# Optimization experiments

Hardware: AMD Instinct MI355X
Metric: run time of the kernel (lower is better)

The kernel has to match this reference:

```python
import jax, jax.numpy as jnp
import numpy as np

DIM, HEADS, MLP_RATIO = 384, 6, 4.0
HEAD_DIM = DIM // HEADS
HID = int(DIM * MLP_RATIO)
EPS = 1e-5


def _layer_norm(x, g, b):
    m = jnp.mean(x, axis=-1, keepdims=True)
    v = jnp.mean(jnp.square(x - m), axis=-1, keepdims=True)
    return (x - m) * jax.lax.rsqrt(v + EPS) * g + b


def setup_inputs() -> dict:
    key = jax.random.key(0)
    ks = jax.random.split(key, 16)
    B, N, C = 4, 2048, DIM
    s = 0.02
    return {
        "x": jax.random.normal(ks[0], (B, N, C), dtype=jnp.float32),
        "ln1_g": jnp.ones((C,), jnp.float32),
        "ln1_b": jnp.zeros((C,), jnp.float32),
        "qkv_w": jax.random.normal(ks[1], (C, 3 * C), jnp.float32) * s,  # [in, out]
        "qkv_b": jnp.zeros((3 * C,), jnp.float32),
        "proj_w": jax.random.normal(ks[2], (C, C), jnp.float32) * s,
        "proj_b": jnp.zeros((C,), jnp.float32),
        "ln2_g": jnp.ones((C,), jnp.float32),
        "ln2_b": jnp.zeros((C,), jnp.float32),
        "fc1_w": jax.random.normal(ks[3], (C, HID), jnp.float32) * s,
        "fc1_b": jnp.zeros((HID,), jnp.float32),
        "fc2_w": jax.random.normal(ks[4], (HID, C), jnp.float32) * s,
        "fc2_b": jnp.zeros((C,), jnp.float32),
    }


def reference(x, ln1_g, ln1_b, qkv_w, qkv_b, proj_w, proj_b,
              ln2_g, ln2_b, fc1_w, fc1_b, fc2_w, fc2_b):
    B, N, C = x.shape
    scale = HEAD_DIM ** (-0.5)

    # --- attention branch (pre-norm) ---
    h = _layer_norm(x, ln1_g, ln1_b)
    qkv = (h @ qkv_w + qkv_b).reshape(B, N, 3, HEADS, HEAD_DIM)
    qkv = jnp.transpose(qkv, (2, 0, 3, 1, 4))  # [3, B, H, N, D]
    q, k, v = qkv[0], qkv[1], qkv[2]
    attn = jnp.einsum("bhnd,bhmd->bhnm", q, k) * scale
    attn = jax.nn.softmax(attn, axis=-1)
    out = jnp.einsum("bhnm,bhmd->bhnd", attn, v)
    out = jnp.transpose(out, (0, 2, 1, 3)).reshape(B, N, C)
    x = x + (out @ proj_w + proj_b)

    # --- MLP branch (pre-norm) ---
    h = _layer_norm(x, ln2_g, ln2_b)
    h = jax.nn.gelu(h @ fc1_w + fc1_b, approximate=False)
    x = x + (h @ fc2_w + fc2_b)
    return x
```

## Files before the change

kernel.cpp:

```cpp
#include <hip/hip_runtime.h>

typedef unsigned short u16;
typedef unsigned int u32;
typedef __bf16 bf16x8_t __attribute__((ext_vector_type(8)));
typedef float f32x4 __attribute__((ext_vector_type(4)));
typedef float f32x16 __attribute__((ext_vector_type(16)));

__device__ __forceinline__ u16 f2b(float f) {
  union { float f; u32 u; } v; v.f = f;
  u32 r = v.u + 0x7fffu + ((v.u >> 16) & 1u);
  return (u16)(r >> 16);
}

__device__ __forceinline__ u32 pkbf(float a, float b) {
  union { __bf16 h[2]; u32 u; } v;
  v.h[0] = (__bf16)a; v.h[1] = (__bf16)b;
  return v.u;
}

__device__ __forceinline__ f32x4 mfma16(uint4 a, uint4 b, f32x4 c) {
  return __builtin_amdgcn_mfma_f32_16x16x32_bf16(
      __builtin_bit_cast(bf16x8_t, a), __builtin_bit_cast(bf16x8_t, b), c, 0, 0, 0);
}

__device__ __forceinline__ f32x16 mfma32(uint4 a, uint4 b, f32x16 c) {
  return __builtin_amdgcn_mfma_f32_32x32x16_bf16(
      __builtin_bit_cast(bf16x8_t, a), __builtin_bit_cast(bf16x8_t, b), c, 0, 0, 0);
}

__device__ __forceinline__ void plswap(u32& a, u32& b) {
  asm("v_permlane32_swap_b32 %0, %1" : "+v"(a), "+v"(b));
}

__device__ __forceinline__ void load_lds16(const void* g, void* l) {
  __builtin_amdgcn_global_load_lds(
      (const __attribute__((address_space(1))) unsigned int*)g,
      (__attribute__((address_space(3))) unsigned int*)l, 16, 0, 0);
}

__global__ __launch_bounds__(256) void convT4_k(
    const float* __restrict__ w0, u16* __restrict__ t0_,
    const float* __restrict__ w1, u16* __restrict__ t1_,
    const float* __restrict__ w2, u16* __restrict__ t2_,
    const float* __restrict__ w3, u16* __restrict__ t3_) {
  __shared__ u16 L[64][68];
  int tile = blockIdx.x, tid = threadIdx.x;
  const float* w; u16* wt; int K, N, rel;
  if (tile < 108)      { w = w0; wt = t0_; K = 384;  N = 1152; rel = tile; }
  else if (tile < 144) { w = w1; wt = t1_; K = 384;  N = 384;  rel = tile - 108; }
  else if (tile < 288) { w = w2; wt = t2_; K = 384;  N = 1536; rel = tile - 144; }
  else                 { w = w3; wt = t3_; K = 1536; N = 384;  rel = tile - 288; }
  int ntx = N >> 6;
  int tk = (rel / ntx) << 6, tn = (rel - (rel / ntx) * ntx) << 6;

  int r = tid >> 2, c0 = (tid & 3) << 4;
  const float* src = w + (size_t)(tk + r) * N + tn + c0;
#pragma unroll
  for (int j = 0; j < 16; j += 4) {
    float4 a = *(const float4*)(src + j);
    L[r][c0 + j + 0] = f2b(a.x);
    L[r][c0 + j + 1] = f2b(a.y);
    L[r][c0 + j + 2] = f2b(a.z);
    L[r][c0 + j + 3] = f2b(a.w);
  }
  __syncthreads();
  int n = tid >> 2, k0 = (tid & 3) << 4;
  u16 tmp[16];
#pragma unroll
  for (int j = 0; j < 16; j++) tmp[j] = L[k0 + j][n];
  u16* dst = wt + (size_t)(tn + n) * K + tk + k0;
  *(uint4*)dst = *(const uint4*)(tmp);
  *(uint4*)(dst + 8) = *(const uint4*)(tmp + 8);
}

__global__ __launch_bounds__(256) void ln_k(const float* __restrict__ x,
                                            const float* __restrict__ g,
                                            const float* __restrict__ bta,
                                            u16* __restrict__ out) {
  int lane = threadIdx.x & 63, wid = threadIdx.x >> 6;
  int row = blockIdx.x * 4 + wid;
  const float* xr = x + (size_t)row * 384;
  float v[6];
  float s = 0.f;
#pragma unroll
  for (int i = 0; i < 6; i++) { v[i] = xr[i * 64 + lane]; s += v[i]; }
#pragma unroll
  for (int off = 32; off >= 1; off >>= 1) s += __shfl_xor(s, off);
  float mean = s * (1.0f / 384.0f);
  float vs = 0.f;
#pragma unroll
  for (int i = 0; i < 6; i++) { float d = v[i] - mean; vs += d * d; }
#pragma unroll
  for (int off = 32; off >= 1; off >>= 1) vs += __shfl_xor(vs, off);
  float rstd = rsqrtf(vs * (1.0f / 384.0f) + 1e-5f);
  u16* orow = out + (size_t)row * 384;
#pragma unroll
  for (int i = 0; i < 6; i++) {
    int c = i * 64 + lane;
    orow[c] = f2b((v[i] - mean) * rstd * g[c] + bta[c]);
  }
}

template <int EPI, int MR>
__global__ __launch_bounds__(256) void gemm_k(
    const u16* __restrict__ A, const u16* __restrict__ Bt,
    const float* __restrict__ bias, const float* __restrict__ res,
    void* __restrict__ outp, int M, int Nn, int K,
    u16* __restrict__ qp, u16* __restrict__ kp, u16* __restrict__ vtp) {
  constexpr int BMt = MR * 32;
  constexpr int AWV = BMt / 32;
  __shared__ __align__(16) u16 As[2][BMt * 64];
  __shared__ __align__(16) u16 Bs[2][64 * 64];
  int tid = threadIdx.x;
  int lane = tid & 63, wid = tid >> 6;
  int li = lane & 15, lg = lane >> 4;
  int wr = wid >> 1, wc = wid & 1;
  int row0 = blockIdx.y * BMt, col0 = blockIdx.x * 64;

  int lr = lane >> 3;
  int sc8 = ((lane & 7) ^ lr) * 8;

  f32x4 z = {0.f, 0.f, 0.f, 0.f};
  f32x4 acc[MR][2];
#pragma unroll
  for (int m = 0; m < MR; m++)
#pragma unroll
    for (int n = 0; n < 2; n++) acc[m][n] = z;

  auto STAGE = [&](int buf, int k0) {
#pragma unroll
    for (int j = 0; j < AWV; j++) {
      int ia = wid * AWV + j;
      load_lds16(A + (size_t)(row0 + ia * 8 + lr) * K + k0 + sc8,
                 (char*)As[buf] + ia * 1024);
    }
#pragma unroll
    for (int j = 0; j < 2; j++) {
      int ib = wid * 2 + j;
      load_lds16(Bt + (size_t)(col0 + ib * 8 + lr) * K + k0 + sc8,
                 (char*)Bs[buf] + ib * 1024);
    }
  };

  int nsteps = K >> 6;
  STAGE(0, 0);

  int buf = 0;
  for (int t = 0; t < nsteps; t++) {
    if (t + 1 < nsteps) {
      STAGE(buf ^ 1, (t + 1) * 64);
      if constexpr (MR == 4)
        asm volatile("s_waitcnt vmcnt(6)" ::: "memory");
      else
        asm volatile("s_waitcnt vmcnt(4)" ::: "memory");
    } else {
      asm volatile("s_waitcnt vmcnt(0)" ::: "memory");
    }
    __builtin_amdgcn_s_barrier();
    asm volatile("" ::: "memory");
    const char* Asb = (const char*)As[buf];
    const char* Bsb = (const char*)Bs[buf];
#pragma unroll
    for (int kk = 0; kk < 2; kk++) {
      uint4 af[MR], bf[2];
#pragma unroll
      for (int m = 0; m < MR; m++) {
        int r = wr * (MR * 16) + m * 16 + li;
        af[m] = *(const uint4*)(Asb + r * 128 +
                                ((kk * 64 + lg * 16) ^ ((r & 7) << 4)));
      }
#pragma unroll
      for (int n = 0; n < 2; n++) {
        int c = wc * 32 + n * 16 + li;
        bf[n] = *(const uint4*)(Bsb + c * 128 +
                                ((kk * 64 + lg * 16) ^ ((c & 7) << 4)));
      }
#pragma unroll
      for (int m = 0; m < MR; m++)
#pragma unroll
        for (int n = 0; n < 2; n++)
          acc[m][n] = mfma16(af[m], bf[n], acc[m][n]);
    }
    asm volatile("" ::: "memory");
    __builtin_amdgcn_s_barrier();
    buf ^= 1;
  }

#pragma unroll
  for (int m = 0; m < MR; m++) {
#pragma unroll
    for (int n = 0; n < 2; n++) {
#pragma unroll
      for (int j = 0; j < 4; j++) {
        int r = row0 + wr * (MR * 16) + m * 16 + lg * 4 + j;
        int c = col0 + wc * 32 + n * 16 + li;
        float v = acc[m][n][j] + bias[c];
        if (EPI == 0) {
          ((float*)outp)[(size_t)r * Nn + c] = v + res[(size_t)r * Nn + c];
        } else if (EPI == 1) {
          float e = __expf(-1.5957691f * v * (1.f + 0.044715f * v * v));
          ((u16*)outp)[(size_t)r * Nn + c] = f2b(v / (1.f + e));
        } else {
          int t = c / 384;
          int c2 = c - t * 384;
          int hh = c2 >> 6, d = c2 & 63;
          int bb = r >> 11, nn = r & 2047;
          size_t bh = (size_t)bb * 6 + hh;
          int tile = nn >> 5;
          if (t == 2) {
            int kvl = nn & 31;
            int kvHalf = (kvl >> 4) & 1, h2 = (kvl >> 3) & 1, jj = kvl & 7;
            int dTile = d >> 5, l31 = d & 31;
            vtp[(((bh * 64 + tile) * 2 + dTile) * 2 + kvHalf) * 512 +
                (l31 + h2 * 32) * 8 + jj] = f2b(v);
          } else {
            int chunk = d >> 4, h2 = (d >> 3) & 1, e = d & 7;
            int l31 = nn & 31;
            size_t off = ((bh * 64 + tile) * 4 + chunk) * 512 +
                         (l31 + h2 * 32) * 8 + e;
            if (t == 0) qp[off] = f2b(v * 0.125f);
            else        kp[off] = f2b(v);
          }
        }
      }
    }
  }
}

__global__ __launch_bounds__(256, 3) void attn_k(const u16* __restrict__ q,
                                                 const u16* __restrict__ k,
                                                 const u16* __restrict__ vt,
                                                 u16* __restrict__ out) {
  __shared__ __align__(16) float Ol[3][2][16][64];
  __shared__ float Ls[3][64];

  int tid = threadIdx.x;
  int lane = tid & 63, wid = tid >> 6;
  int l31 = lane & 31, hi = lane >> 5;
  int bid = blockIdx.x;
  int nid = (bid & 7) * 192 + (bid >> 3);
  int bh = nid >> 6, qTile = nid & 63;
  int b = bh / 6, hh = bh - b * 6;
  int qb = qTile * 32;

  const u16* qp_ = q + (size_t)(bh * 64 + qTile) * 2048 + lane * 8;
  const u16* kp_ = k + (size_t)(bh * 64 + wid * 16) * 2048 + lane * 8;
  const u16* vp_ = vt + (size_t)(bh * 64 + wid * 16) * 2048 + lane * 8;

  uint4 qf[4], kf[4];
#pragma unroll
  for (int c = 0; c < 4; c++) qf[c] = *(const uint4*)(qp_ + c * 512);
#pragma unroll
  for (int c = 0; c < 4; c++) kf[c] = *(const uint4*)(kp_ + c * 512);
  kp_ += 2048;

  f32x16 o0, o1;
#pragma unroll
  for (int r = 0; r < 16; r++) { o0[r] = 0.f; o1[r] = 0.f; }
  float lsum = 0.f;

#pragma unroll
  for (int t = 0; t < 16; t++) {
    uint4 vf0 = *(const uint4*)(vp_);
    uint4 vf1 = *(const uint4*)(vp_ + 512);
    uint4 vf2 = *(const uint4*)(vp_ + 1024);
    uint4 vf3 = *(const uint4*)(vp_ + 1536);
    uint4 kn[4];
    if (t < 15) {
#pragma unroll
      for (int c = 0; c < 4; c++) kn[c] = *(const uint4*)(kp_ + c * 512);
    }

    f32x16 s;
#pragma unroll
    for (int r = 0; r < 16; r++) s[r] = 0.f;
    s = mfma32(kf[0], qf[0], s);
    s = mfma32(kf[1], qf[1], s);
    s = mfma32(kf[2], qf[2], s);
    s = mfma32(kf[3], qf[3], s);

    float p[16];
#pragma unroll
    for (int r = 0; r < 16; r++) p[r] = __expf(s[r]);

    float a0 = (p[0] + p[1]) + (p[2] + p[3]);
    float a1 = (p[4] + p[5]) + (p[6] + p[7]);
    float a2 = (p[8] + p[9]) + (p[10] + p[11]);
    float a3 = (p[12] + p[13]) + (p[14] + p[15]);
    lsum += (a0 + a1) + (a2 + a3);

    u32 u[8];
#pragma unroll
    for (int i = 0; i < 8; i++) u[i] = pkbf(p[2 * i], p[2 * i + 1]);
    plswap(u[0], u[2]); plswap(u[1], u[3]);
    plswap(u[4], u[6]); plswap(u[5], u[7]);
    uint4 pa0 = {u[0], u[1], u[2], u[3]};
    uint4 pa1 = {u[4], u[5], u[6], u[7]};

    o0 = mfma32(pa0, vf0, o0);
    o0 = mfma32(pa1, vf1, o0);
    o1 = mfma32(pa0, vf2, o1);
    o1 = mfma32(pa1, vf3, o1);

    if (t < 15) {
#pragma unroll
      for (int c = 0; c < 4; c++) kf[c] = kn[c];
    }
    kp_ += 2048;
    vp_ += 2048;
  }

  lsum += __shfl_xor(lsum, 32);

  if (wid) {
#pragma unroll
    for (int r = 0; r < 16; r++) {
      Ol[wid - 1][0][r][lane] = o0[r];
      Ol[wid - 1][1][r][lane] = o1[r];
    }
    Ls[wid - 1][lane] = lsum;
  }
  __syncthreads();
  if (wid == 0) {
#pragma unroll
    for (int w = 0; w < 3; w++) lsum += Ls[w][lane];
#pragma unroll
    for (int r = 0; r < 16; r++)
#pragma unroll
      for (int w = 0; w < 3; w++) {
        o0[r] += Ol[w][0][r][lane];
        o1[r] += Ol[w][1][r][lane];
      }
    float rl = 1.0f / lsum;
#pragma unroll
    for (int r = 0; r < 16; r++) {
      int qo = (r & 3) + 8 * (r >> 2) + hi * 4;
      float rlq = __shfl(rl, qo, 64);
      int row = b * 2048 + qb + qo;
      out[(size_t)row * 384 + hh * 64 + l31] = f2b(o0[r] * rlq);
      out[(size_t)row * 384 + hh * 64 + 32 + l31] = f2b(o1[r] * rlq);
    }
  }
}

extern "C" void kernel_launch(void* const* d_in, const int* in_sizes, int n_in,
                              void* d_out, int out_size, void* d_ws,
                              size_t ws_size, hipStream_t stream) {
  const float* x      = (const float*)d_in[0];
  const float* ln1_g  = (const float*)d_in[1];
  const float* ln1_b  = (const float*)d_in[2];
  const float* qkv_w  = (const float*)d_in[3];
  const float* qkv_b  = (const float*)d_in[4];
  const float* proj_w = (const float*)d_in[5];
  const float* proj_b = (const float*)d_in[6];
  const float* ln2_g  = (const float*)d_in[7];
  const float* ln2_b  = (const float*)d_in[8];
  const float* fc1_w  = (const float*)d_in[9];
  const float* fc1_b  = (const float*)d_in[10];
  const float* fc2_w  = (const float*)d_in[11];
  const float* fc2_b  = (const float*)d_in[12];
  float* out = (float*)d_out;

  char* p = (char*)d_ws;
  u16* qkvwt  = (u16*)p;  p += (size_t)1152 * 384 * 2;
  u16* projwt = (u16*)p;  p += (size_t)384 * 384 * 2;
  u16* fc1wt  = (u16*)p;  p += (size_t)1536 * 384 * 2;
  u16* fc2wt  = (u16*)p;  p += (size_t)384 * 1536 * 2;
  float* x1   = (float*)p; p += (size_t)8192 * 384 * 4;
  u16* reg1   = (u16*)p;  p += (size_t)8192 * 384 * 2;
  u16* reg2   = (u16*)p;  p += (size_t)8192 * 1536 * 2;
  u16* qd  = reg2;
  u16* kd  = reg2 + (size_t)24 * 2048 * 64;
  u16* vtd = kd + (size_t)24 * 2048 * 64;
  u16* h3  = reg2;

  convT4_k<<<432, 256, 0, stream>>>(qkv_w, qkvwt, proj_w, projwt,
                                    fc1_w, fc1wt, fc2_w, fc2wt);

  ln_k<<<2048, 256, 0, stream>>>(x, ln1_g, ln1_b, reg1);
  gemm_k<2, 4><<<dim3(18, 64), 256, 0, stream>>>(
      reg1, qkvwt, qkv_b, nullptr, nullptr, 8192, 1152, 384, qd, kd, vtd);
  attn_k<<<dim3(1536), 256, 0, stream>>>(qd, kd, vtd, reg1);
  gemm_k<0, 2><<<dim3(6, 128), 256, 0, stream>>>(
      reg1, projwt, proj_b, x, x1, 8192, 384, 384, nullptr, nullptr, nullptr);
  ln_k<<<2048, 256, 0, stream>>>(x1, ln2_g, ln2_b, reg1);
  gemm_k<1, 4><<<dim3(24, 64), 256, 0, stream>>>(
      reg1, fc1wt, fc1_b, nullptr, h3, 8192, 1536, 384, nullptr, nullptr, nullptr);
  gemm_k<0, 2><<<dim3(6, 128), 256, 0, stream>>>(
      h3, fc2wt, fc2_b, x1, out, 8192, 384, 1536, nullptr, nullptr, nullptr);
}
```

Before: 140.1 us.

## Widen GEMM N-tiles and process two query tiles per attention block

The GEMM kernel gains an NR template parameter, so the QKV and FC1 GEMMs now use 128x128 tiles instead of 128x64, halving the grid width and the re-reading of A. The attention kernel now handles 64 queries per block (two 32-row tiles) sharing each K/V fragment load, and K and V are prefetched together. It also switches exp to exp2 by folding log2(e) into the Q scale. In exchange the kernels use more registers and drop attention occupancy from 3 to 2 blocks per SM, and the output reduction through shared memory runs twice with extra barriers.

```diff
diff --git a/kernel.cpp b/kernel.cpp
--- a/kernel.cpp
+++ b/kernel.cpp
@@ -36,6 +36,14 @@
   __builtin_amdgcn_global_load_lds(
       (const __attribute__((address_space(1))) unsigned int*)g,
       (__attribute__((address_space(3))) unsigned int*)l, 16, 0, 0);
+}
+
+template <int N>
+__device__ __forceinline__ void waitvm() {
+  if constexpr (N == 0) asm volatile("s_waitcnt vmcnt(0)" ::: "memory");
+  else if constexpr (N == 4) asm volatile("s_waitcnt vmcnt(4)" ::: "memory");
+  else if constexpr (N == 6) asm volatile("s_waitcnt vmcnt(6)" ::: "memory");
+  else asm volatile("s_waitcnt vmcnt(8)" ::: "memory");
 }
 
 __global__ __launch_bounds__(256) void convT4_k(
@@ -101,42 +109,42 @@
   }
 }
 
-template <int EPI, int MR>
+template <int EPI, int MR, int NR>
 __global__ __launch_bounds__(256) void gemm_k(
     const u16* __restrict__ A, const u16* __restrict__ Bt,
     const float* __restrict__ bias, const float* __restrict__ res,
     void* __restrict__ outp, int M, int Nn, int K,
     u16* __restrict__ qp, u16* __restrict__ kp, u16* __restrict__ vtp) {
   constexpr int BMt = MR * 32;
-  constexpr int AWV = BMt / 32;
+  constexpr int BNt = NR * 32;
   __shared__ __align__(16) u16 As[2][BMt * 64];
-  __shared__ __align__(16) u16 Bs[2][64 * 64];
+  __shared__ __align__(16) u16 Bs[2][BNt * 64];
   int tid = threadIdx.x;
   int lane = tid & 63, wid = tid >> 6;
   int li = lane & 15, lg = lane >> 4;
   int wr = wid >> 1, wc = wid & 1;
-  int row0 = blockIdx.y * BMt, col0 = blockIdx.x * 64;
+  int row0 = blockIdx.y * BMt, col0 = blockIdx.x * BNt;
 
   int lr = lane >> 3;
   int sc8 = ((lane & 7) ^ lr) * 8;
 
   f32x4 z = {0.f, 0.f, 0.f, 0.f};
-  f32x4 acc[MR][2];
+  f32x4 acc[MR][NR];
 #pragma unroll
   for (int m = 0; m < MR; m++)
 #pragma unroll
-    for (int n = 0; n < 2; n++) acc[m][n] = z;
+    for (int n = 0; n < NR; n++) acc[m][n] = z;
 
   auto STAGE = [&](int buf, int k0) {
 #pragma unroll
-    for (int j = 0; j < AWV; j++) {
-      int ia = wid * AWV + j;
+    for (int j = 0; j < MR; j++) {
+      int ia = wid * MR + j;
       load_lds16(A + (size_t)(row0 + ia * 8 + lr) * K + k0 + sc8,
                  (char*)As[buf] + ia * 1024);
     }
 #pragma unroll
-    for (int j = 0; j < 2; j++) {
-      int ib = wid * 2 + j;
+    for (int j = 0; j < NR; j++) {
+      int ib = wid * NR + j;
       load_lds16(Bt + (size_t)(col0 + ib * 8 + lr) * K + k0 + sc8,
                  (char*)Bs[buf] + ib * 1024);
     }
@@ -149,12 +157,9 @@
   for (int t = 0; t < nsteps; t++) {
     if (t + 1 < nsteps) {
       STAGE(buf ^ 1, (t + 1) * 64);
-      if constexpr (MR == 4)
-        asm volatile("s_waitcnt vmcnt(6)" ::: "memory");
-      else
-        asm volatile("s_waitcnt vmcnt(4)" ::: "memory");
+      waitvm<MR + NR>();
     } else {
-      asm volatile("s_waitcnt vmcnt(0)" ::: "memory");
+      waitvm<0>();
     }
     __builtin_amdgcn_s_barrier();
     asm volatile("" ::: "memory");
@@ -162,7 +167,7 @@
     const char* Bsb = (const char*)Bs[buf];
 #pragma unroll
     for (int kk = 0; kk < 2; kk++) {
-      uint4 af[MR], bf[2];
+      uint4 af[MR], bf[NR];
 #pragma unroll
       for (int m = 0; m < MR; m++) {
         int r = wr * (MR * 16) + m * 16 + li;
@@ -170,15 +175,15 @@
                                 ((kk * 64 + lg * 16) ^ ((r & 7) << 4)));
       }
 #pragma unroll
-      for (int n = 0; n < 2; n++) {
-        int c = wc * 32 + n * 16 + li;
+      for (int n = 0; n < NR; n++) {
+        int c = wc * (NR * 16) + n * 16 + li;
         bf[n] = *(const uint4*)(Bsb + c * 128 +
                                 ((kk * 64 + lg * 16) ^ ((c & 7) << 4)));
       }
 #pragma unroll
       for (int m = 0; m < MR; m++)
 #pragma unroll
-        for (int n = 0; n < 2; n++)
+        for (int n = 0; n < NR; n++)
           acc[m][n] = mfma16(af[m], bf[n], acc[m][n]);
     }
     asm volatile("" ::: "memory");
@@ -189,11 +194,11 @@
 #pragma unroll
   for (int m = 0; m < MR; m++) {
 #pragma unroll
-    for (int n = 0; n < 2; n++) {
+    for (int n = 0; n < NR; n++) {
 #pragma unroll
       for (int j = 0; j < 4; j++) {
         int r = row0 + wr * (MR * 16) + m * 16 + lg * 4 + j;
-        int c = col0 + wc * 32 + n * 16 + li;
+        int c = col0 + wc * (NR * 16) + n * 16 + li;
         float v = acc[m][n][j] + bias[c];
         if (EPI == 0) {
           ((float*)outp)[(size_t)r * Nn + c] = v + res[(size_t)r * Nn + c];
@@ -218,7 +223,7 @@
             int l31 = nn & 31;
             size_t off = ((bh * 64 + tile) * 4 + chunk) * 512 +
                          (l31 + h2 * 32) * 8 + e;
-            if (t == 0) qp[off] = f2b(v * 0.125f);
+            if (t == 0) qp[off] = f2b(v * 0.18033688f);
             else        kp[off] = f2b(v);
           }
         }
@@ -227,7 +232,7 @@
   }
 }
 
-__global__ __launch_bounds__(256, 3) void attn_k(const u16* __restrict__ q,
+__global__ __launch_bounds__(256, 2) void attn_k(const u16* __restrict__ q,
                                                  const u16* __restrict__ k,
                                                  const u16* __restrict__ vt,
                                                  u16* __restrict__ out) {
@@ -238,107 +243,155 @@
   int lane = tid & 63, wid = tid >> 6;
   int l31 = lane & 31, hi = lane >> 5;
   int bid = blockIdx.x;
-  int nid = (bid & 7) * 192 + (bid >> 3);
-  int bh = nid >> 6, qTile = nid & 63;
+  int nid = (bid & 7) * 96 + (bid >> 3);
+  int bh = nid >> 5, qT = nid & 31;
   int b = bh / 6, hh = bh - b * 6;
-  int qb = qTile * 32;
-
-  const u16* qp_ = q + (size_t)(bh * 64 + qTile) * 2048 + lane * 8;
-  const u16* kp_ = k + (size_t)(bh * 64 + wid * 16) * 2048 + lane * 8;
-  const u16* vp_ = vt + (size_t)(bh * 64 + wid * 16) * 2048 + lane * 8;
-
-  uint4 qf[4], kf[4];
-#pragma unroll
-  for (int c = 0; c < 4; c++) qf[c] = *(const uint4*)(qp_ + c * 512);
+  int qb = qT * 64;
+
+  const u16* qp_ = q + ((size_t)bh * 64 + qT * 2) * 2048 + lane * 8;
+  const u16* kp_ = k + ((size_t)bh * 64 + wid * 16) * 2048 + lane * 8;
+  const u16* vp_ = vt + ((size_t)bh * 64 + wid * 16) * 2048 + lane * 8;
+
+  uint4 qf0[4], qf1[4], kf[4], vf[4];
+#pragma unroll
+  for (int c = 0; c < 4; c++) qf0[c] = *(const uint4*)(qp_ + c * 512);
+#pragma unroll
+  for (int c = 0; c < 4; c++) qf1[c] = *(const uint4*)(qp_ + 2048 + c * 512);
 #pragma unroll
   for (int c = 0; c < 4; c++) kf[c] = *(const uint4*)(kp_ + c * 512);
+#pragma unroll
+  for (int c = 0; c < 4; c++) vf[c] = *(const uint4*)(vp_ + c * 512);
   kp_ += 2048;
-
-  f32x16 o0, o1;
-#pragma unroll
-  for (int r = 0; r < 16; r++) { o0[r] = 0.f; o1[r] = 0.f; }
-  float lsum = 0.f;
+  vp_ += 2048;
+
+  f32x16 o00, o01, o10, o11;
+#pragma unroll
+  for (int r = 0; r < 16; r++) { o00[r] = 0.f; o01[r] = 0.f; o10[r] = 0.f; o11[r] = 0.f; }
+  float ls0 = 0.f, ls1 = 0.f;
 
 #pragma unroll
   for (int t = 0; t < 16; t++) {
-    uint4 vf0 = *(const uint4*)(vp_);
-    uint4 vf1 = *(const uint4*)(vp_ + 512);
-    uint4 vf2 = *(const uint4*)(vp_ + 1024);
-    uint4 vf3 = *(const uint4*)(vp_ + 1536);
-    uint4 kn[4];
+    uint4 kn[4], vn[4];
     if (t < 15) {
 #pragma unroll
       for (int c = 0; c < 4; c++) kn[c] = *(const uint4*)(kp_ + c * 512);
-    }
-
-    f32x16 s;
-#pragma unroll
-    for (int r = 0; r < 16; r++) s[r] = 0.f;
-    s = mfma32(kf[0], qf[0], s);
-    s = mfma32(kf[1], qf[1], s);
-    s = mfma32(kf[2], qf[2], s);
-    s = mfma32(kf[3], qf[3], s);
-
-    float p[16];
-#pragma unroll
-    for (int r = 0; r < 16; r++) p[r] = __expf(s[r]);
-
-    float a0 = (p[0] + p[1]) + (p[2] + p[3]);
-    float a1 = (p[4] + p[5]) + (p[6] + p[7]);
-    float a2 = (p[8] + p[9]) + (p[10] + p[11]);
-    float a3 = (p[12] + p[13]) + (p[14] + p[15]);
-    lsum += (a0 + a1) + (a2 + a3);
-
-    u32 u[8];
-#pragma unroll
-    for (int i = 0; i < 8; i++) u[i] = pkbf(p[2 * i], p[2 * i + 1]);
-    plswap(u[0], u[2]); plswap(u[1], u[3]);
-    plswap(u[4], u[6]); plswap(u[5], u[7]);
-    uint4 pa0 = {u[0], u[1], u[2], u[3]};
-    uint4 pa1 = {u[4], u[5], u[6], u[7]};
-
-    o0 = mfma32(pa0, vf0, o0);
-    o0 = mfma32(pa1, vf1, o0);
-    o1 = mfma32(pa0, vf2, o1);
-    o1 = mfma32(pa1, vf3, o1);
+#pragma unroll
+      for (int c = 0; c < 4; c++) vn[c] = *(const uint4*)(vp_ + c * 512);
+    }
+
+    f32x16 s0, s1;
+#pragma unroll
+    for (int r = 0; r < 16; r++) { s0[r] = 0.f; s1[r] = 0.f; }
+#pragma unroll
+    for (int c = 0; c < 4; c++) s0 = mfma32(kf[c], qf0[c], s0);
+#pragma unroll
+    for (int c = 0; c < 4; c++) s1 = mfma32(kf[c], qf1[c], s1);
+
+    {
+      float p[16];
+#pragma unroll
+      for (int r = 0; r < 16; r++) p[r] = __builtin_amdgcn_exp2f(s0[r]);
+      ls0 += ((p[0] + p[1]) + (p[2] + p[3])) + ((p[4] + p[5]) + (p[6] + p[7])) +
+             ((p[8] + p[9]) + (p[10] + p[11])) + ((p[12] + p[13]) + (p[14] + p[15]));
+      u32 u[8];
+#pragma unroll
+      for (int i = 0; i < 8; i++) u[i] = pkbf(p[2 * i], p[2 * i + 1]);
+      plswap(u[0], u[2]); plswap(u[1], u[3]);
+      plswap(u[4], u[6]); plswap(u[5], u[7]);
+      uint4 pa0 = {u[0], u[1], u[2], u[3]};
+      uint4 pa1 = {u[4], u[5], u[6], u[7]};
+      o00 = mfma32(pa0, vf[0], o00);
+      o00 = mfma32(pa1, vf[1], o00);
+      o01 = mfma32(pa0, vf[2], o01);
+      o01 = mfma32(pa1, vf[3], o01);
+    }
+    {
+      float p[16];
+#pragma unroll
+      for (int r = 0; r < 16; r++) p[r] = __builtin_amdgcn_exp2f(s1[r]);
+      ls1 += ((p[0] + p[1]) + (p[2] + p[3])) + ((p[4] + p[5]) + (p[6] + p[7])) +
+             ((p[8] + p[9]) + (p[10] + p[11])) + ((p[12] + p[13]) + (p[14] + p[15]));
+      u32 u[8];
+#pragma unroll
+      for (int i = 0; i < 8; i++) u[i] = pkbf(p[2 * i], p[2 * i + 1]);
+      plswap(u[0], u[2]); plswap(u[1], u[3]);
+      plswap(u[4], u[6]); plswap(u[5], u[7]);
+      uint4 pa0 = {u[0], u[1], u[2], u[3]};
+      uint4 pa1 = {u[4], u[5], u[6], u[7]};
+      o10 = mfma32(pa0, vf[0], o10);
+      o10 = mfma32(pa1, vf[1], o10);
+      o11 = mfma32(pa0, vf[2], o11);
+      o11 = mfma32(pa1, vf[3], o11);
+    }
 
     if (t < 15) {
 #pragma unroll
-      for (int c = 0; c < 4; c++) kf[c] = kn[c];
+      for (int c = 0; c < 4; c++) { kf[c] = kn[c]; vf[c] = vn[c]; }
     }
     kp_ += 2048;
     vp_ += 2048;
   }
 
-  lsum += __shfl_xor(lsum, 32);
+  ls0 += __shfl_xor(ls0, 32);
+  ls1 += __shfl_xor(ls1, 32);
 
   if (wid) {
 #pragma unroll
     for (int r = 0; r < 16; r++) {
-      Ol[wid - 1][0][r][lane] = o0[r];
-      Ol[wid - 1][1][r][lane] = o1[r];
-    }
-    Ls[wid - 1][lane] = lsum;
+      Ol[wid - 1][0][r][lane] = o00[r];
+      Ol[wid - 1][1][r][lane] = o01[r];
+    }
+    Ls[wid - 1][lane] = ls0;
   }
   __syncthreads();
   if (wid == 0) {
 #pragma unroll
-    for (int w = 0; w < 3; w++) lsum += Ls[w][lane];
+    for (int w = 0; w < 3; w++) ls0 += Ls[w][lane];
 #pragma unroll
     for (int r = 0; r < 16; r++)
 #pragma unroll
       for (int w = 0; w < 3; w++) {
-        o0[r] += Ol[w][0][r][lane];
-        o1[r] += Ol[w][1][r][lane];
+        o00[r] += Ol[w][0][r][lane];
+        o01[r] += Ol[w][1][r][lane];
       }
-    float rl = 1.0f / lsum;
+    float rl = 1.0f / ls0;
 #pragma unroll
     for (int r = 0; r < 16; r++) {
       int qo = (r & 3) + 8 * (r >> 2) + hi * 4;
       float rlq = __shfl(rl, qo, 64);
       int row = b * 2048 + qb + qo;
-      out[(size_t)row * 384 + hh * 64 + l31] = f2b(o0[r] * rlq);
-      out[(size_t)row * 384 + hh * 64 + 32 + l31] = f2b(o1[r] * rlq);
+      out[(size_t)row * 384 + hh * 64 + l31] = f2b(o00[r] * rlq);
+      out[(size_t)row * 384 + hh * 64 + 32 + l31] = f2b(o01[r] * rlq);
+    }
+  }
+  __syncthreads();
+  if (wid) {
+#pragma unroll
+    for (int r = 0; r < 16; r++) {
+      Ol[wid - 1][0][r][lane] = o10[r];
+      Ol[wid - 1][1][r][lane] = o11[r];
+    }
+    Ls[wid - 1][lane] = ls1;
+  }
+  __syncthreads();
+  if (wid == 0) {
+#pragma unroll
+    for (int w = 0; w < 3; w++) ls1 += Ls[w][lane];
+#pragma unroll
+    for (int r = 0; r < 16; r++)
+#pragma unroll
+      for (int w = 0; w < 3; w++) {
+        o10[r] += Ol[w][0][r][lane];
+        o11[r] += Ol[w][1][r][lane];
+      }
+    float rl = 1.0f / ls1;
+#pragma unroll
+    for (int r = 0; r < 16; r++) {
+      int qo = (r & 3) + 8 * (r >> 2) + hi * 4;
+      float rlq = __shfl(rl, qo, 64);
+      int row = b * 2048 + qb + 32 + qo;
+      out[(size_t)row * 384 + hh * 64 + l31] = f2b(o10[r] * rlq);
+      out[(size_t)row * 384 + hh * 64 + 32 + l31] = f2b(o11[r] * rlq);
     }
   }
 }
@@ -378,14 +431,14 @@
                                     fc1_w, fc1wt, fc2_w, fc2wt);
 
   ln_k<<<2048, 256, 0, stream>>>(x, ln1_g, ln1_b, reg1);
-  gemm_k<2, 4><<<dim3(18, 64), 256, 0, stream>>>(
+  gemm_k<2, 4, 4><<<dim3(9, 64), 256, 0, stream>>>(
       reg1, qkvwt, qkv_b, nullptr, nullptr, 8192, 1152, 384, qd, kd, vtd);
-  attn_k<<<dim3(1536), 256, 0, stream>>>(qd, kd, vtd, reg1);
-  gemm_k<0, 2><<<dim3(6, 128), 256, 0, stream>>>(
+  attn_k<<<dim3(768), 256, 0, stream>>>(qd, kd, vtd, reg1);
+  gemm_k<0, 2, 2><<<dim3(6, 128), 256, 0, stream>>>(
       reg1, projwt, proj_b, x, x1, 8192, 384, 384, nullptr, nullptr, nullptr);
   ln_k<<<2048, 256, 0, stream>>>(x1, ln2_g, ln2_b, reg1);
-  gemm_k<1, 4><<<dim3(24, 64), 256, 0, stream>>>(
+  gemm_k<1, 4, 4><<<dim3(12, 64), 256, 0, stream>>>(
       reg1, fc1wt, fc1_b, nullptr, h3, 8192, 1536, 384, nullptr, nullptr, nullptr);
-  gemm_k<0, 2><<<dim3(6, 128), 256, 0, stream>>>(
+  gemm_k<0, 2, 2><<<dim3(6, 128), 256, 0, stream>>>(
       h3, fc2wt, fc2_b, x1, out, 8192, 384, 1536, nullptr, nullptr, nullptr);
 }
```

Result: no change. 142.5 us (+1.8%).
